# Optimization experiments

Hardware: AMD Instinct MI355X
Metric: run time of the kernel (lower is better)

The kernel has to match this reference:

```python
import jax, jax.numpy as jnp
import numpy as np

N_WORD_IDS, N_TAG_IDS, N_DEPREL_IDS = 100000, 48, 40
N_WORD_F, N_TAG_F, N_DEPREL_F = 18, 18, 12
EMBED, HIDDEN, N_CLASSES = 128, 1024, 3
B = 16384
N_TOTAL = N_WORD_F + N_TAG_F + N_DEPREL_F  # 48


def _he(key, shape):
    fan_in = shape[0]
    return jax.random.normal(key, shape, dtype=jnp.float32) * jnp.sqrt(2.0 / fan_in)


def setup_inputs() -> dict:
    key = jax.random.key(0)
    ks = jax.random.split(key, 8)
    return {
        "word_id_batch": jax.random.randint(ks[0], (B, N_WORD_F), 0, N_WORD_IDS, dtype=jnp.int64 if jax.config.jax_enable_x64 else jnp.int32).astype(jnp.int32),
        "tag_id_batch": jax.random.randint(ks[1], (B, N_TAG_F), 0, N_TAG_IDS).astype(jnp.int32),
        "deprel_id_batch": jax.random.randint(ks[2], (B, N_DEPREL_F), 0, N_DEPREL_IDS).astype(jnp.int32),
        "word_embeddings": jax.random.normal(ks[3], (N_WORD_IDS, EMBED), dtype=jnp.float32) * 0.1,
        "tag_embeddings": _he(ks[4], (N_TAG_IDS, EMBED)),
        "deprel_embeddings": _he(ks[5], (N_DEPREL_IDS, EMBED)),
        "W_h": _he(ks[6], (N_TOTAL * EMBED, HIDDEN)),
        "b_h": jnp.zeros((HIDDEN,), jnp.float32),
        "W_o": _he(ks[7], (HIDDEN, N_CLASSES)),
        "b_o": jnp.zeros((N_CLASSES,), jnp.float32),
    }


def reference(word_id_batch, tag_id_batch, deprel_id_batch,
              word_embeddings, tag_embeddings, deprel_embeddings,
              W_h, b_h, W_o, b_o):
    # one_hot_float(ids) @ E is mathematically a row gather: E[ids]
    b = word_id_batch.shape[0]
    x = jnp.concatenate([
        word_embeddings[word_id_batch].reshape(b, -1),      # (B, 18*E)
        tag_embeddings[tag_id_batch].reshape(b, -1),        # (B, 18*E)
        deprel_embeddings[deprel_id_batch].reshape(b, -1),  # (B, 12*E)
    ], axis=1)                                              # (B, 48*E)
    h = jax.nn.relu(x @ W_h + b_h)
    # dropout is identity in eval mode (self.training == False)
    return h @ W_o + b_o
```

## Files before the change

### kernel.cpp

```cpp
#include <hip/hip_runtime.h>
#include <hip/hip_bf16.h>
#include <cstdint>

typedef unsigned short u16;
typedef __attribute__((ext_vector_type(8))) short bf16x8;
typedef __attribute__((ext_vector_type(4))) float f32x4;

#define B_ROWS 16384
#define N_HID  1024
#define K_DIM  6144
#define EMB    128
#define N_WORD 100000
#define N_TAG  48
#define N_DEP  40
#define NTILES 96
#define NITER  48

__device__ __forceinline__ u16 f2bf(float x) {
  union { float f; uint32_t u; } v; v.f = x;
  uint32_t r = v.u + 0x7fffu + ((v.u >> 16) & 1u);
  return (u16)(r >> 16);
}

__device__ __forceinline__ void gload_lds16(const void* g, void* l) {
  __builtin_amdgcn_global_load_lds(
      (const __attribute__((address_space(1))) void*)g,
      (__attribute__((address_space(3))) void*)l, 16, 0, 0);
}

#define SBAR do { \
  __builtin_amdgcn_sched_barrier(0); \
  asm volatile("" ::: "memory"); \
  __builtin_amdgcn_s_barrier(); \
  asm volatile("" ::: "memory"); \
  __builtin_amdgcn_sched_barrier(0); \
} while (0)

__global__ void init_out_kernel(float* __restrict__ out, const float* __restrict__ b_o) {
  int i = blockIdx.x * blockDim.x + threadIdx.x;
  if (i < B_ROWS * 3) out[i] = b_o[i % 3];
}

__global__ void transpose_wh_kernel(const float* __restrict__ Wh, u16* __restrict__ Wt) {
  __shared__ float tile[32][33];
  int k0 = blockIdx.x * 32, n0 = blockIdx.y * 32;
  int tx = threadIdx.x & 31, ty = threadIdx.x >> 5;
  #pragma unroll
  for (int j = 0; j < 4; ++j)
    tile[ty + j * 8][tx] = Wh[(size_t)(k0 + ty + j * 8) * N_HID + n0 + tx];
  __syncthreads();
  #pragma unroll
  for (int j = 0; j < 4; ++j)
    Wt[(size_t)(n0 + ty + j * 8) * K_DIM + k0 + tx] = f2bf(tile[tx][ty + j * 8]);
}

__global__ void cast_tables_kernel(const float* __restrict__ wordE, const float* __restrict__ tagE,
                                   const float* __restrict__ depE, u16* __restrict__ tblB) {
  const int W8 = N_WORD * EMB / 8, T8 = N_TAG * EMB / 8, D8 = N_DEP * EMB / 8;
  int i = blockIdx.x * blockDim.x + threadIdx.x;
  const float* src; int j;
  if (i < W8)                { src = wordE; j = i; }
  else if (i < W8 + T8)      { src = tagE;  j = i - W8; }
  else if (i < W8 + T8 + D8) { src = depE;  j = i - W8 - T8; }
  else return;
  const float4* s = (const float4*)(src + (size_t)j * 8);
  float4 v0 = s[0], v1 = s[1];
  bf16x8 w;
  w[0] = (short)f2bf(v0.x); w[1] = (short)f2bf(v0.y);
  w[2] = (short)f2bf(v0.z); w[3] = (short)f2bf(v0.w);
  w[4] = (short)f2bf(v1.x); w[5] = (short)f2bf(v1.y);
  w[6] = (short)f2bf(v1.z); w[7] = (short)f2bf(v1.w);
  *(bf16x8*)(tblB + (size_t)i * 8) = w;
}

__global__ void build_offv_kernel(const int* __restrict__ w, const int* __restrict__ t,
                                  const int* __restrict__ d, int* __restrict__ offv) {
  int row = blockIdx.x * 256 + threadIdx.x;
  int f = blockIdx.y;
  if (row >= B_ROWS) return;
  int off;
  if (f < 18)      off = w[row * 18 + f] * EMB;
  else if (f < 36) off = N_WORD * EMB + t[row * 18 + (f - 18)] * EMB;
  else             off = (N_WORD + N_TAG) * EMB + d[row * 12 + (f - 36)] * EMB;
  offv[f * B_ROWS + row] = off;
}

__device__ __forceinline__ void rd_b4(const u16* base, int sch, bf16x8* q) {
  #pragma unroll
  for (int nf = 0; nf < 4; ++nf) q[nf] = *(const bf16x8*)(base + nf * 1024 + sch);
}
__device__ __forceinline__ void rd_a4(const u16* base, int sch, int mh, bf16x8* q) {
  #pragma unroll
  for (int mf = 0; mf < 4; ++mf) q[mf] = *(const bf16x8*)(base + (mh * 4 + mf) * 1024 + sch);
}
__device__ __forceinline__ void mfma16(f32x4 (&acc)[8][4], int mh, const bf16x8* aT, const bf16x8* bq) {
  #pragma unroll
  for (int m = 0; m < 4; ++m)
    #pragma unroll
    for (int n = 0; n < 4; ++n)
      acc[mh * 4 + m][n] = __builtin_amdgcn_mfma_f32_16x16x32_bf16(aT[m], bq[n], acc[mh * 4 + m][n], 0, 0, 0);
}

__global__ __launch_bounds__(512, 2) void fused_v3_kernel(
    const u16* __restrict__ tblB, const int* __restrict__ offv,
    const u16* __restrict__ Wt,   const float* __restrict__ b_h,
    const float* __restrict__ W_o, float* __restrict__ out) {
  __shared__ u16 As[2][256 * 64];
  __shared__ u16 Bs[2][256 * 64];

  const int tid  = threadIdx.x;
  const int lane = tid & 63;
  const int wid  = tid >> 6;
  const int wr   = wid >> 2;
  const int wc   = wid & 3;
  const int bn0  = blockIdx.x * 256;
  const int bm0  = blockIdx.y * 256;
  const int l15  = lane & 15, ca = lane >> 4;

  const int r0 = tid >> 3;
  const int c  = tid & 7;
  const int sc = ((c ^ (r0 & 7)) << 3);
  const u16* Bp[4];
  #pragma unroll
  for (int j = 0; j < 4; ++j)
    Bp[j] = Wt + (size_t)(bn0 + j * 64 + r0) * K_DIM + sc;
  const int ivb = bm0 + r0;

#define DESTA(buf, h, is) ((void*)&As[buf][(h) * 8192 + (is) * 4096 + wid * 512])
#define DESTB(buf, h, is) ((void*)&Bs[buf][(h) * 8192 + (is) * 4096 + wid * 512])
#define STAGE_B2(buf, h, t) do { \
    gload_lds16(Bp[2 * (h)] + (size_t)(t) * 64, DESTB(buf, h, 0)); \
    gload_lds16(Bp[2 * (h) + 1] + (size_t)(t) * 64, DESTB(buf, h, 1)); } while (0)
#define STAGE_A2(buf, h, e0) do { \
    gload_lds16(tblB + (size_t)oA[2 * (h)] + (e0) + sc, DESTA(buf, h, 0)); \
    gload_lds16(tblB + (size_t)oA[2 * (h) + 1] + (e0) + sc, DESTA(buf, h, 1)); } while (0)

  const u16* aBase0 = &As[0][(wr * 128 + l15) * 64];
  const u16* aBase1 = &As[1][(wr * 128 + l15) * 64];
  const u16* bBase0 = &Bs[0][(wc * 64 + l15) * 64];
  const u16* bBase1 = &Bs[1][(wc * 64 + l15) * 64];
  const int sch0 = ((ca    ) ^ (l15 & 7)) << 3;
  const int sch1 = ((ca + 4) ^ (l15 & 7)) << 3;

  f32x4 acc[8][4] = {};
  int oA[4];

  STAGE_B2(0, 0, 0); STAGE_B2(0, 1, 0);
  #pragma unroll
  for (int j = 0; j < 4; ++j) oA[j] = offv[ivb + j * 64];
  STAGE_A2(0, 0, 0); STAGE_A2(0, 1, 0);
  STAGE_B2(1, 0, 1); STAGE_B2(1, 1, 1);
  asm volatile("s_waitcnt vmcnt(4)" ::: "memory");
  SBAR;

  #pragma unroll 1
  for (int i = 0; i < NITER; ++i) {
    const int T = 2 * i;
    bf16x8 bq0[4], bq1[4], aT[4];
    rd_b4(bBase0, sch0, bq0);
    rd_a4(aBase0, sch0, 0, aT);
    STAGE_A2(1, 0, 64);
    SBAR;
    __builtin_amdgcn_s_setprio(1); mfma16(acc, 0, aT, bq0); __builtin_amdgcn_s_setprio(0);
    SBAR;
    rd_b4(bBase0, sch1, bq1);
    rd_a4(aBase0, sch0, 1, aT);
    STAGE_A2(1, 1, 64);
    SBAR;
    __builtin_amdgcn_s_setprio(1); mfma16(acc, 1, aT, bq0); __builtin_amdgcn_s_setprio(0);
    SBAR;
    if (i + 1 < NITER) {
      const int* ov = offv + (i + 1) * B_ROWS + ivb;
      #pragma unroll
      for (int j = 0; j < 4; ++j) oA[j] = ov[j * 64];
    }
    rd_a4(aBase0, sch1, 0, aT);
    if (T + 2 < NTILES) STAGE_B2(0, 0, T + 2);
    SBAR;
    __builtin_amdgcn_s_setprio(1); mfma16(acc, 0, aT, bq1); __builtin_amdgcn_s_setprio(0);
    SBAR;
    rd_a4(aBase0, sch1, 1, aT);
    if (T + 2 < NTILES) STAGE_B2(0, 1, T + 2);
    if (i == NITER - 1) { asm volatile("s_waitcnt vmcnt(0)" ::: "memory"); }
    else                { asm volatile("s_waitcnt vmcnt(8)" ::: "memory"); }
    SBAR;
    __builtin_amdgcn_s_setprio(1); mfma16(acc, 1, aT, bq1); __builtin_amdgcn_s_setprio(0);
    SBAR;
    rd_b4(bBase1, sch0, bq0);
    rd_a4(aBase1, sch0, 0, aT);
    if (T + 2 < NTILES) STAGE_A2(0, 0, 0);
    SBAR;
    __builtin_amdgcn_s_setprio(1); mfma16(acc, 0, aT, bq0); __builtin_amdgcn_s_setprio(0);
    SBAR;
    rd_b4(bBase1, sch1, bq1);
    rd_a4(aBase1, sch0, 1, aT);
    if (T + 2 < NTILES) STAGE_A2(0, 1, 0);
    SBAR;
    __builtin_amdgcn_s_setprio(1); mfma16(acc, 1, aT, bq0); __builtin_amdgcn_s_setprio(0);
    SBAR;
    rd_a4(aBase1, sch1, 0, aT);
    if (T + 3 < NTILES) STAGE_B2(1, 0, T + 3);
    SBAR;
    __builtin_amdgcn_s_setprio(1); mfma16(acc, 0, aT, bq1); __builtin_amdgcn_s_setprio(0);
    SBAR;
    rd_a4(aBase1, sch1, 1, aT);
    if (T + 3 < NTILES) STAGE_B2(1, 1, T + 3);
    asm volatile("s_waitcnt vmcnt(4)" ::: "memory");
    SBAR;
    __builtin_amdgcn_s_setprio(1); mfma16(acc, 1, aT, bq1); __builtin_amdgcn_s_setprio(0);
    SBAR;
  }

  float bh[4], wo[4][3];
  #pragma unroll
  for (int nf = 0; nf < 4; ++nf) {
    int j = bn0 + wc * 64 + nf * 16 + l15;
    bh[nf] = b_h[j];
    wo[nf][0] = W_o[j * 3 + 0]; wo[nf][1] = W_o[j * 3 + 1]; wo[nf][2] = W_o[j * 3 + 2];
  }
  #pragma unroll
  for (int mf = 0; mf < 8; ++mf) {
    #pragma unroll
    for (int reg = 0; reg < 4; ++reg) {
      float p0 = 0.f, p1 = 0.f, p2 = 0.f;
      #pragma unroll
      for (int nf = 0; nf < 4; ++nf) {
        float h = acc[mf][nf][reg] + bh[nf];
        h = fmaxf(h, 0.f);
        p0 += h * wo[nf][0]; p1 += h * wo[nf][1]; p2 += h * wo[nf][2];
      }
      #pragma unroll
      for (int mask = 1; mask < 16; mask <<= 1) {
        p0 += __shfl_xor(p0, mask);
        p1 += __shfl_xor(p1, mask);
        p2 += __shfl_xor(p2, mask);
      }
      if (l15 == 0) {
        int row = bm0 + wr * 128 + mf * 16 + (ca << 2) + reg;
        atomicAdd(&out[row * 3 + 0], p0);
        atomicAdd(&out[row * 3 + 1], p1);
        atomicAdd(&out[row * 3 + 2], p2);
      }
    }
  }
#undef DESTA
#undef DESTB
#undef STAGE_B2
#undef STAGE_A2
}

__global__ __launch_bounds__(256, 4) void fused_v2_kernel(
    const int* __restrict__ word_ids, const int* __restrict__ tag_ids,
    const int* __restrict__ dep_ids,  const u16* __restrict__ tblB,
    const u16* __restrict__ Wt,       const float* __restrict__ b_h,
    const float* __restrict__ W_o,    float* __restrict__ out) {
  __shared__ u16 As2[128 * 64];
  __shared__ u16 Bs2[128 * 64];
  const int tid  = threadIdx.x;
  const int lane = tid & 63;
  const int wid  = tid >> 6;
  const int wr   = wid >> 1, wc = wid & 1;
  const int bm0  = blockIdx.y * 128;
  const int bn0  = blockIdx.x * 128;
  f32x4 acc[4][4] = {};

  for (int kt = 0; kt < K_DIM / 64; ++kt) {
    __syncthreads();
    {
      int f = kt >> 1, e0 = (kt & 1) << 6;
      const int* ids; int nf, fl; size_t tb;
      if (f < 18)      { ids = word_ids; nf = 18; fl = f;      tb = 0; }
      else if (f < 36) { ids = tag_ids;  nf = 18; fl = f - 18; tb = (size_t)N_WORD * EMB; }
      else             { ids = dep_ids;  nf = 12; fl = f - 36; tb = (size_t)(N_WORD + N_TAG) * EMB; }
      #pragma unroll
      for (int it = 0; it < 4; ++it) {
        int cidx = wid * 256 + it * 64 + lane;
        int r = cidx >> 3, cc = cidx & 7;
        int id = ids[(bm0 + r) * nf + fl];
        const u16* src = tblB + tb + (size_t)id * EMB + e0 + ((cc ^ (r & 7)) << 3);
        gload_lds16(src, &As2[(wid * 256 + it * 64) * 8]);
      }
    }
    #pragma unroll
    for (int it = 0; it < 4; ++it) {
      int cidx = wid * 256 + it * 64 + lane;
      int rn = cidx >> 3, cc = cidx & 7;
      const u16* src = Wt + (size_t)(bn0 + rn) * K_DIM + kt * 64 + ((cc ^ (rn & 7)) << 3);
      gload_lds16(src, &Bs2[(wid * 256 + it * 64) * 8]);
    }
    __syncthreads();
    const int l15 = lane & 15, ca = lane >> 4;
    #pragma unroll
    for (int ks = 0; ks < 2; ++ks) {
      bf16x8 a[4], b[4];
      #pragma unroll
      for (int m = 0; m < 4; ++m) {
        int ra = wr * 64 + m * 16 + l15;
        int ch = (ca + ks * 4) ^ (ra & 7);
        a[m] = *(const bf16x8*)&As2[ra * 64 + ch * 8];
      }
      #pragma unroll
      for (int n = 0; n < 4; ++n) {
        int rb = wc * 64 + n * 16 + l15;
        int ch = (ca + ks * 4) ^ (rb & 7);
        b[n] = *(const bf16x8*)&Bs2[rb * 64 + ch * 8];
      }
      #pragma unroll
      for (int m = 0; m < 4; ++m)
        #pragma unroll
        for (int n = 0; n < 4; ++n)
          acc[m][n] = __builtin_amdgcn_mfma_f32_16x16x32_bf16(a[m], b[n], acc[m][n], 0, 0, 0);
    }
  }

  const int l15 = lane & 15;
  float bh[4], wo[4][3];
  #pragma unroll
  for (int n = 0; n < 4; ++n) {
    int j = bn0 + wc * 64 + n * 16 + l15;
    bh[n] = b_h[j];
    wo[n][0] = W_o[j * 3 + 0]; wo[n][1] = W_o[j * 3 + 1]; wo[n][2] = W_o[j * 3 + 2];
  }
  #pragma unroll
  for (int m = 0; m < 4; ++m) {
    #pragma unroll
    for (int reg = 0; reg < 4; ++reg) {
      float p0 = 0.f, p1 = 0.f, p2 = 0.f;
      #pragma unroll
      for (int n = 0; n < 4; ++n) {
        float h = acc[m][n][reg] + bh[n];
        h = fmaxf(h, 0.f);
        p0 += h * wo[n][0]; p1 += h * wo[n][1]; p2 += h * wo[n][2];
      }
      #pragma unroll
      for (int mask = 1; mask < 16; mask <<= 1) {
        p0 += __shfl_xor(p0, mask);
        p1 += __shfl_xor(p1, mask);
        p2 += __shfl_xor(p2, mask);
      }
      if (l15 == 0) {
        int row = bm0 + wr * 64 + m * 16 + ((lane >> 4) << 2) + reg;
        atomicAdd(&out[row * 3 + 0], p0);
        atomicAdd(&out[row * 3 + 1], p1);
        atomicAdd(&out[row * 3 + 2], p2);
      }
    }
  }
}

extern "C" void kernel_launch(void* const* d_in, const int* in_sizes, int n_in,
                              void* d_out, int out_size, void* d_ws, size_t ws_size,
                              hipStream_t stream) {
  const int*   word_ids = (const int*)d_in[0];
  const int*   tag_ids  = (const int*)d_in[1];
  const int*   dep_ids  = (const int*)d_in[2];
  const float* wordE    = (const float*)d_in[3];
  const float* tagE     = (const float*)d_in[4];
  const float* depE     = (const float*)d_in[5];
  const float* Wh       = (const float*)d_in[6];
  const float* b_h      = (const float*)d_in[7];
  const float* W_o      = (const float*)d_in[8];
  const float* b_o      = (const float*)d_in[9];
  float*       out      = (float*)d_out;

  const size_t WT_ELEMS  = (size_t)N_HID * K_DIM;
  const size_t TBL_ELEMS = (size_t)(N_WORD + N_TAG + N_DEP) * EMB;
  const size_t OFFV_ELEMS = (size_t)48 * B_ROWS;
  const size_t NEED_V2 = (WT_ELEMS + TBL_ELEMS) * sizeof(u16);
  const size_t NEED_V3 = NEED_V2 + OFFV_ELEMS * sizeof(int);

  u16* Wt   = (u16*)d_ws;
  u16* tblB = Wt + WT_ELEMS;
  int* offv = (int*)(tblB + TBL_ELEMS);

  init_out_kernel<<<(B_ROWS * 3 + 255) / 256, 256, 0, stream>>>(out, b_o);

  if (d_ws && ws_size >= NEED_V3) {
    transpose_wh_kernel<<<dim3(K_DIM / 32, N_HID / 32), 256, 0, stream>>>(Wh, Wt);
    cast_tables_kernel<<<(int)((TBL_ELEMS / 8 + 255) / 256), 256, 0, stream>>>(wordE, tagE, depE, tblB);
    build_offv_kernel<<<dim3(B_ROWS / 256, 48), 256, 0, stream>>>(word_ids, tag_ids, dep_ids, offv);
    fused_v3_kernel<<<dim3(N_HID / 256, B_ROWS / 256), 512, 0, stream>>>(
        tblB, offv, Wt, b_h, W_o, out);
  } else if (d_ws && ws_size >= NEED_V2) {
    transpose_wh_kernel<<<dim3(K_DIM / 32, N_HID / 32), 256, 0, stream>>>(Wh, Wt);
    cast_tables_kernel<<<(int)((TBL_ELEMS / 8 + 255) / 256), 256, 0, stream>>>(wordE, tagE, depE, tblB);
    fused_v2_kernel<<<dim3(N_HID / 128, B_ROWS / 128), 256, 0, stream>>>(
        word_ids, tag_ids, dep_ids, tblB, Wt, b_h, W_o, out);
  }
}
```

Measured before the change: 325.1 us.

## Switch fused GEMM to 32x32x16 MFMA with register double-buffered LDS reads

Replaces the 16x16x32 bf16 MFMA tiling with 32x32x16 MFMA (4x2 fragments per wave), which halves the number of LDS fragment reads per unit of compute and issues fewer, larger matrix instructions. The pipeline is restructured so LDS fragment reads for the next k-slice are double-buffered in registers while the current MFMAs run, and A and B global staging for the next tile are issued together. The epilogue is adapted to the 32x32 output layout, with wider shuffle reductions. Risks include higher register pressure and a less staggered global prefetch with a full vmcnt(0) wait each iteration.

Measured after the change: 381.3 us. 1.17x slower.

```diff
diff --git a/kernel.cpp b/kernel.cpp
--- a/kernel.cpp
+++ b/kernel.cpp
@@ -5,6 +5,7 @@
 typedef unsigned short u16;
 typedef __attribute__((ext_vector_type(8))) short bf16x8;
 typedef __attribute__((ext_vector_type(4))) float f32x4;
+typedef __attribute__((ext_vector_type(16))) float f32x16;
 
 #define B_ROWS 16384
 #define N_HID  1024
@@ -85,23 +86,7 @@
   offv[f * B_ROWS + row] = off;
 }
 
-__device__ __forceinline__ void rd_b4(const u16* base, int sch, bf16x8* q) {
-  #pragma unroll
-  for (int nf = 0; nf < 4; ++nf) q[nf] = *(const bf16x8*)(base + nf * 1024 + sch);
-}
-__device__ __forceinline__ void rd_a4(const u16* base, int sch, int mh, bf16x8* q) {
-  #pragma unroll
-  for (int mf = 0; mf < 4; ++mf) q[mf] = *(const bf16x8*)(base + (mh * 4 + mf) * 1024 + sch);
-}
-__device__ __forceinline__ void mfma16(f32x4 (&acc)[8][4], int mh, const bf16x8* aT, const bf16x8* bq) {
-  #pragma unroll
-  for (int m = 0; m < 4; ++m)
-    #pragma unroll
-    for (int n = 0; n < 4; ++n)
-      acc[mh * 4 + m][n] = __builtin_amdgcn_mfma_f32_16x16x32_bf16(aT[m], bq[n], acc[mh * 4 + m][n], 0, 0, 0);
-}
-
-__global__ __launch_bounds__(512, 2) void fused_v3_kernel(
+__global__ __launch_bounds__(512, 2) void fused_v4_kernel(
     const u16* __restrict__ tblB, const int* __restrict__ offv,
     const u16* __restrict__ Wt,   const float* __restrict__ b_h,
     const float* __restrict__ W_o, float* __restrict__ out) {
@@ -115,7 +100,7 @@
   const int wc   = wid & 3;
   const int bn0  = blockIdx.x * 256;
   const int bm0  = blockIdx.y * 256;
-  const int l15  = lane & 15, ca = lane >> 4;
+  const int l31  = lane & 31, lh = lane >> 5;
 
   const int r0 = tid >> 3;
   const int c  = tid & 7;
@@ -135,108 +120,113 @@
     gload_lds16(tblB + (size_t)oA[2 * (h)] + (e0) + sc, DESTA(buf, h, 0)); \
     gload_lds16(tblB + (size_t)oA[2 * (h) + 1] + (e0) + sc, DESTA(buf, h, 1)); } while (0)
 
-  const u16* aBase0 = &As[0][(wr * 128 + l15) * 64];
-  const u16* aBase1 = &As[1][(wr * 128 + l15) * 64];
-  const u16* bBase0 = &Bs[0][(wc * 64 + l15) * 64];
-  const u16* bBase1 = &Bs[1][(wc * 64 + l15) * 64];
-  const int sch0 = ((ca    ) ^ (l15 & 7)) << 3;
-  const int sch1 = ((ca + 4) ^ (l15 & 7)) << 3;
-
-  f32x4 acc[8][4] = {};
+  const u16* aB[2] = { &As[0][(wr * 128 + l31) * 64], &As[1][(wr * 128 + l31) * 64] };
+  const u16* bB[2] = { &Bs[0][(wc * 64  + l31) * 64], &Bs[1][(wc * 64  + l31) * 64] };
+  int sch[4];
+  #pragma unroll
+  for (int ks = 0; ks < 4; ++ks) sch[ks] = (((ks * 2 + lh) ^ (lane & 7)) << 3);
+
+#define RD(Aset, Bset, buf, ks) do { \
+    _Pragma("unroll") for (int mf = 0; mf < 4; ++mf) \
+      Aset[mf] = *(const bf16x8*)(aB[buf] + mf * 2048 + sch[ks]); \
+    _Pragma("unroll") for (int nf = 0; nf < 2; ++nf) \
+      Bset[nf] = *(const bf16x8*)(bB[buf] + nf * 2048 + sch[ks]); } while (0)
+
+#define MM(Aset, Bset) do { \
+    __builtin_amdgcn_s_setprio(1); \
+    _Pragma("unroll") for (int mf = 0; mf < 4; ++mf) \
+      _Pragma("unroll") for (int nf = 0; nf < 2; ++nf) \
+        acc[mf][nf] = __builtin_amdgcn_mfma_f32_32x32x16_bf16(Aset[mf], Bset[nf], acc[mf][nf], 0, 0, 0); \
+    __builtin_amdgcn_s_setprio(0); } while (0)
+
+  f32x16 acc[4][2] = {};
   int oA[4];
+  bf16x8 A0[4], A1[4], B0[2], B1[2];
 
   STAGE_B2(0, 0, 0); STAGE_B2(0, 1, 0);
   #pragma unroll
   for (int j = 0; j < 4; ++j) oA[j] = offv[ivb + j * 64];
   STAGE_A2(0, 0, 0); STAGE_A2(0, 1, 0);
-  STAGE_B2(1, 0, 1); STAGE_B2(1, 1, 1);
-  asm volatile("s_waitcnt vmcnt(4)" ::: "memory");
+  asm volatile("s_waitcnt vmcnt(0)" ::: "memory");
   SBAR;
+  RD(A0, B0, 0, 0);
 
   #pragma unroll 1
   for (int i = 0; i < NITER; ++i) {
     const int T = 2 * i;
-    bf16x8 bq0[4], bq1[4], aT[4];
-    rd_b4(bBase0, sch0, bq0);
-    rd_a4(aBase0, sch0, 0, aT);
-    STAGE_A2(1, 0, 64);
-    SBAR;
-    __builtin_amdgcn_s_setprio(1); mfma16(acc, 0, aT, bq0); __builtin_amdgcn_s_setprio(0);
-    SBAR;
-    rd_b4(bBase0, sch1, bq1);
-    rd_a4(aBase0, sch0, 1, aT);
-    STAGE_A2(1, 1, 64);
-    SBAR;
-    __builtin_amdgcn_s_setprio(1); mfma16(acc, 1, aT, bq0); __builtin_amdgcn_s_setprio(0);
-    SBAR;
-    if (i + 1 < NITER) {
+    const bool more = (i + 1 < NITER);
+    RD(A1, B1, 0, 1);
+    STAGE_A2(1, 0, 64); STAGE_B2(1, 0, T + 1);
+    SBAR;
+    MM(A0, B0);
+    SBAR;
+    RD(A0, B0, 0, 2);
+    STAGE_A2(1, 1, 64); STAGE_B2(1, 1, T + 1);
+    SBAR;
+    MM(A1, B1);
+    SBAR;
+    if (more) {
       const int* ov = offv + (i + 1) * B_ROWS + ivb;
       #pragma unroll
       for (int j = 0; j < 4; ++j) oA[j] = ov[j * 64];
     }
-    rd_a4(aBase0, sch1, 0, aT);
-    if (T + 2 < NTILES) STAGE_B2(0, 0, T + 2);
-    SBAR;
-    __builtin_amdgcn_s_setprio(1); mfma16(acc, 0, aT, bq1); __builtin_amdgcn_s_setprio(0);
-    SBAR;
-    rd_a4(aBase0, sch1, 1, aT);
-    if (T + 2 < NTILES) STAGE_B2(0, 1, T + 2);
+    RD(A1, B1, 0, 3);
+    SBAR;
+    MM(A0, B0);
+    SBAR;
     if (i == NITER - 1) { asm volatile("s_waitcnt vmcnt(0)" ::: "memory"); }
-    else                { asm volatile("s_waitcnt vmcnt(8)" ::: "memory"); }
-    SBAR;
-    __builtin_amdgcn_s_setprio(1); mfma16(acc, 1, aT, bq1); __builtin_amdgcn_s_setprio(0);
-    SBAR;
-    rd_b4(bBase1, sch0, bq0);
-    rd_a4(aBase1, sch0, 0, aT);
-    if (T + 2 < NTILES) STAGE_A2(0, 0, 0);
-    SBAR;
-    __builtin_amdgcn_s_setprio(1); mfma16(acc, 0, aT, bq0); __builtin_amdgcn_s_setprio(0);
-    SBAR;
-    rd_b4(bBase1, sch1, bq1);
-    rd_a4(aBase1, sch0, 1, aT);
-    if (T + 2 < NTILES) STAGE_A2(0, 1, 0);
-    SBAR;
-    __builtin_amdgcn_s_setprio(1); mfma16(acc, 1, aT, bq0); __builtin_amdgcn_s_setprio(0);
-    SBAR;
-    rd_a4(aBase1, sch1, 0, aT);
-    if (T + 3 < NTILES) STAGE_B2(1, 0, T + 3);
-    SBAR;
-    __builtin_amdgcn_s_setprio(1); mfma16(acc, 0, aT, bq1); __builtin_amdgcn_s_setprio(0);
-    SBAR;
-    rd_a4(aBase1, sch1, 1, aT);
-    if (T + 3 < NTILES) STAGE_B2(1, 1, T + 3);
-    asm volatile("s_waitcnt vmcnt(4)" ::: "memory");
-    SBAR;
-    __builtin_amdgcn_s_setprio(1); mfma16(acc, 1, aT, bq1); __builtin_amdgcn_s_setprio(0);
-    SBAR;
-  }
-
-  float bh[4], wo[4][3];
-  #pragma unroll
-  for (int nf = 0; nf < 4; ++nf) {
-    int j = bn0 + wc * 64 + nf * 16 + l15;
+    else                { asm volatile("s_waitcnt vmcnt(4)" ::: "memory"); }
+    SBAR;
+    RD(A0, B0, 1, 0);
+    MM(A1, B1);
+    SBAR;
+    RD(A1, B1, 1, 1);
+    if (more) { STAGE_A2(0, 0, 0); STAGE_B2(0, 0, T + 2); }
+    SBAR;
+    MM(A0, B0);
+    SBAR;
+    RD(A0, B0, 1, 2);
+    if (more) { STAGE_A2(0, 1, 0); STAGE_B2(0, 1, T + 2); }
+    SBAR;
+    MM(A1, B1);
+    SBAR;
+    RD(A1, B1, 1, 3);
+    SBAR;
+    MM(A0, B0);
+    SBAR;
+    if (more) { asm volatile("s_waitcnt vmcnt(0)" ::: "memory"); }
+    SBAR;
+    if (more) RD(A0, B0, 0, 0);
+    MM(A1, B1);
+    SBAR;
+  }
+
+  float bh[2], wo[2][3];
+  #pragma unroll
+  for (int nf = 0; nf < 2; ++nf) {
+    int j = bn0 + wc * 64 + nf * 32 + l31;
     bh[nf] = b_h[j];
     wo[nf][0] = W_o[j * 3 + 0]; wo[nf][1] = W_o[j * 3 + 1]; wo[nf][2] = W_o[j * 3 + 2];
   }
   #pragma unroll
-  for (int mf = 0; mf < 8; ++mf) {
+  for (int mf = 0; mf < 4; ++mf) {
     #pragma unroll
-    for (int reg = 0; reg < 4; ++reg) {
+    for (int reg = 0; reg < 16; ++reg) {
       float p0 = 0.f, p1 = 0.f, p2 = 0.f;
       #pragma unroll
-      for (int nf = 0; nf < 4; ++nf) {
+      for (int nf = 0; nf < 2; ++nf) {
         float h = acc[mf][nf][reg] + bh[nf];
         h = fmaxf(h, 0.f);
         p0 += h * wo[nf][0]; p1 += h * wo[nf][1]; p2 += h * wo[nf][2];
       }
       #pragma unroll
-      for (int mask = 1; mask < 16; mask <<= 1) {
+      for (int mask = 1; mask < 32; mask <<= 1) {
         p0 += __shfl_xor(p0, mask);
         p1 += __shfl_xor(p1, mask);
         p2 += __shfl_xor(p2, mask);
       }
-      if (l15 == 0) {
-        int row = bm0 + wr * 128 + mf * 16 + (ca << 2) + reg;
+      if (l31 == 0) {
+        int row = bm0 + wr * 128 + mf * 32 + (reg & 3) + 8 * (reg >> 2) + 4 * lh;
         atomicAdd(&out[row * 3 + 0], p0);
         atomicAdd(&out[row * 3 + 1], p1);
         atomicAdd(&out[row * 3 + 2], p2);
@@ -247,6 +237,8 @@
 #undef DESTB
 #undef STAGE_B2
 #undef STAGE_A2
+#undef RD
+#undef MM
 }
 
 __global__ __launch_bounds__(256, 4) void fused_v2_kernel(
@@ -363,11 +355,11 @@
   const float* b_o      = (const float*)d_in[9];
   float*       out      = (float*)d_out;
 
-  const size_t WT_ELEMS  = (size_t)N_HID * K_DIM;
-  const size_t TBL_ELEMS = (size_t)(N_WORD + N_TAG + N_DEP) * EMB;
+  const size_t WT_ELEMS   = (size_t)N_HID * K_DIM;
+  const size_t TBL_ELEMS  = (size_t)(N_WORD + N_TAG + N_DEP) * EMB;
   const size_t OFFV_ELEMS = (size_t)48 * B_ROWS;
   const size_t NEED_V2 = (WT_ELEMS + TBL_ELEMS) * sizeof(u16);
-  const size_t NEED_V3 = NEED_V2 + OFFV_ELEMS * sizeof(int);
+  const size_t NEED_V4 = NEED_V2 + OFFV_ELEMS * sizeof(int);
 
   u16* Wt   = (u16*)d_ws;
   u16* tblB = Wt + WT_ELEMS;
@@ -375,11 +367,11 @@
 
   init_out_kernel<<<(B_ROWS * 3 + 255) / 256, 256, 0, stream>>>(out, b_o);
 
-  if (d_ws && ws_size >= NEED_V3) {
+  if (d_ws && ws_size >= NEED_V4) {
     transpose_wh_kernel<<<dim3(K_DIM / 32, N_HID / 32), 256, 0, stream>>>(Wh, Wt);
     cast_tables_kernel<<<(int)((TBL_ELEMS / 8 + 255) / 256), 256, 0, stream>>>(wordE, tagE, depE, tblB);
     build_offv_kernel<<<dim3(B_ROWS / 256, 48), 256, 0, stream>>>(word_ids, tag_ids, dep_ids, offv);
-    fused_v3_kernel<<<dim3(N_HID / 256, B_ROWS / 256), 512, 0, stream>>>(
+    fused_v4_kernel<<<dim3(N_HID / 256, B_ROWS / 256), 512, 0, stream>>>(
         tblB, offv, Wt, b_h, W_o, out);
   } else if (d_ws && ws_size >= NEED_V2) {
     transpose_wh_kernel<<<dim3(K_DIM / 32, N_HID / 32), 256, 0, stream>>>(Wh, Wt);
```

## Software-pipeline LDS fragment reads and reschedule global staging in fused GEMM loop

Applied to the files above, without the earlier changes.

Restructures the main K loop so LDS-to-register fragment reads for the next MFMA block use double register sets (aT0/aT1, bq0/bq1) and are issued before the current MFMAs. B tiles are now staged together with A tiles, and the waitcnt placement changes accordingly. Launch bounds drop to one block per SIMD set, which frees registers for the extra fragments but may lower occupancy. The aim is to hide LDS read latency behind MFMA work, at the cost of more register pressure and a changed global-load overlap depth.

Result: slower. 528.8 us (+62.6%).

```diff
diff --git a/kernel.cpp b/kernel.cpp
--- a/kernel.cpp
+++ b/kernel.cpp
@@ -94,14 +94,16 @@
   for (int mf = 0; mf < 4; ++mf) q[mf] = *(const bf16x8*)(base + (mh * 4 + mf) * 1024 + sch);
 }
 __device__ __forceinline__ void mfma16(f32x4 (&acc)[8][4], int mh, const bf16x8* aT, const bf16x8* bq) {
+  __builtin_amdgcn_s_setprio(1);
   #pragma unroll
   for (int m = 0; m < 4; ++m)
     #pragma unroll
     for (int n = 0; n < 4; ++n)
       acc[mh * 4 + m][n] = __builtin_amdgcn_mfma_f32_16x16x32_bf16(aT[m], bq[n], acc[mh * 4 + m][n], 0, 0, 0);
-}
-
-__global__ __launch_bounds__(512, 2) void fused_v3_kernel(
+  __builtin_amdgcn_s_setprio(0);
+}
+
+__global__ __launch_bounds__(512, 1) void fused_v5_kernel(
     const u16* __restrict__ tblB, const int* __restrict__ offv,
     const u16* __restrict__ Wt,   const float* __restrict__ b_h,
     const float* __restrict__ W_o, float* __restrict__ out) {
@@ -144,70 +146,70 @@
 
   f32x4 acc[8][4] = {};
   int oA[4];
+  bf16x8 aT0[4], aT1[4], bq0[4], bq1[4];
 
   STAGE_B2(0, 0, 0); STAGE_B2(0, 1, 0);
   #pragma unroll
   for (int j = 0; j < 4; ++j) oA[j] = offv[ivb + j * 64];
   STAGE_A2(0, 0, 0); STAGE_A2(0, 1, 0);
-  STAGE_B2(1, 0, 1); STAGE_B2(1, 1, 1);
-  asm volatile("s_waitcnt vmcnt(4)" ::: "memory");
+  asm volatile("s_waitcnt vmcnt(0)" ::: "memory");
   SBAR;
+  rd_b4(bBase0, sch0, bq0);
+  rd_a4(aBase0, sch0, 0, aT0);
 
   #pragma unroll 1
   for (int i = 0; i < NITER; ++i) {
     const int T = 2 * i;
-    bf16x8 bq0[4], bq1[4], aT[4];
-    rd_b4(bBase0, sch0, bq0);
-    rd_a4(aBase0, sch0, 0, aT);
-    STAGE_A2(1, 0, 64);
-    SBAR;
-    __builtin_amdgcn_s_setprio(1); mfma16(acc, 0, aT, bq0); __builtin_amdgcn_s_setprio(0);
-    SBAR;
+    const bool more = (i + 1 < NITER);
+    rd_a4(aBase0, sch0, 1, aT1);
     rd_b4(bBase0, sch1, bq1);
-    rd_a4(aBase0, sch0, 1, aT);
-    STAGE_A2(1, 1, 64);
-    SBAR;
-    __builtin_amdgcn_s_setprio(1); mfma16(acc, 1, aT, bq0); __builtin_amdgcn_s_setprio(0);
-    SBAR;
-    if (i + 1 < NITER) {
+    STAGE_A2(1, 0, 64); STAGE_B2(1, 0, T + 1);
+    SBAR;
+    mfma16(acc, 0, aT0, bq0);
+    SBAR;
+    rd_a4(aBase0, sch1, 0, aT0);
+    STAGE_A2(1, 1, 64); STAGE_B2(1, 1, T + 1);
+    SBAR;
+    mfma16(acc, 1, aT1, bq0);
+    SBAR;
+    rd_a4(aBase0, sch1, 1, aT1);
+    if (more) {
       const int* ov = offv + (i + 1) * B_ROWS + ivb;
       #pragma unroll
       for (int j = 0; j < 4; ++j) oA[j] = ov[j * 64];
     }
-    rd_a4(aBase0, sch1, 0, aT);
-    if (T + 2 < NTILES) STAGE_B2(0, 0, T + 2);
-    SBAR;
-    __builtin_amdgcn_s_setprio(1); mfma16(acc, 0, aT, bq1); __builtin_amdgcn_s_setprio(0);
-    SBAR;
-    rd_a4(aBase0, sch1, 1, aT);
-    if (T + 2 < NTILES) STAGE_B2(0, 1, T + 2);
-    if (i == NITER - 1) { asm volatile("s_waitcnt vmcnt(0)" ::: "memory"); }
-    else                { asm volatile("s_waitcnt vmcnt(8)" ::: "memory"); }
-    SBAR;
-    __builtin_amdgcn_s_setprio(1); mfma16(acc, 1, aT, bq1); __builtin_amdgcn_s_setprio(0);
+    SBAR;
+    mfma16(acc, 0, aT0, bq1);
+    SBAR;
+    if (more) { asm volatile("s_waitcnt vmcnt(4)" ::: "memory"); }
+    else      { asm volatile("s_waitcnt vmcnt(0)" ::: "memory"); }
     SBAR;
     rd_b4(bBase1, sch0, bq0);
-    rd_a4(aBase1, sch0, 0, aT);
-    if (T + 2 < NTILES) STAGE_A2(0, 0, 0);
-    SBAR;
-    __builtin_amdgcn_s_setprio(1); mfma16(acc, 0, aT, bq0); __builtin_amdgcn_s_setprio(0);
-    SBAR;
+    rd_a4(aBase1, sch0, 0, aT0);
+    mfma16(acc, 1, aT1, bq1);
+    SBAR;
+    rd_a4(aBase1, sch0, 1, aT1);
     rd_b4(bBase1, sch1, bq1);
-    rd_a4(aBase1, sch0, 1, aT);
-    if (T + 2 < NTILES) STAGE_A2(0, 1, 0);
-    SBAR;
-    __builtin_amdgcn_s_setprio(1); mfma16(acc, 1, aT, bq0); __builtin_amdgcn_s_setprio(0);
-    SBAR;
-    rd_a4(aBase1, sch1, 0, aT);
-    if (T + 3 < NTILES) STAGE_B2(1, 0, T + 3);
-    SBAR;
-    __builtin_amdgcn_s_setprio(1); mfma16(acc, 0, aT, bq1); __builtin_amdgcn_s_setprio(0);
-    SBAR;
-    rd_a4(aBase1, sch1, 1, aT);
-    if (T + 3 < NTILES) STAGE_B2(1, 1, T + 3);
-    asm volatile("s_waitcnt vmcnt(4)" ::: "memory");
-    SBAR;
-    __builtin_amdgcn_s_setprio(1); mfma16(acc, 1, aT, bq1); __builtin_amdgcn_s_setprio(0);
+    if (more) { STAGE_A2(0, 0, 0); STAGE_B2(0, 0, T + 2); }
+    SBAR;
+    mfma16(acc, 0, aT0, bq0);
+    SBAR;
+    rd_a4(aBase1, sch1, 0, aT0);
+    if (more) { STAGE_A2(0, 1, 0); STAGE_B2(0, 1, T + 2); }
+    SBAR;
+    mfma16(acc, 1, aT1, bq0);
+    SBAR;
+    rd_a4(aBase1, sch1, 1, aT1);
+    SBAR;
+    mfma16(acc, 0, aT0, bq1);
+    SBAR;
+    if (more) { asm volatile("s_waitcnt vmcnt(0)" ::: "memory"); }
+    SBAR;
+    if (more) {
+      rd_b4(bBase0, sch0, bq0);
+      rd_a4(aBase0, sch0, 0, aT0);
+    }
+    mfma16(acc, 1, aT1, bq1);
     SBAR;
   }
 
@@ -363,11 +365,11 @@
   const float* b_o      = (const float*)d_in[9];
   float*       out      = (float*)d_out;
 
-  const size_t WT_ELEMS  = (size_t)N_HID * K_DIM;
-  const size_t TBL_ELEMS = (size_t)(N_WORD + N_TAG + N_DEP) * EMB;
+  const size_t WT_ELEMS   = (size_t)N_HID * K_DIM;
+  const size_t TBL_ELEMS  = (size_t)(N_WORD + N_TAG + N_DEP) * EMB;
   const size_t OFFV_ELEMS = (size_t)48 * B_ROWS;
   const size_t NEED_V2 = (WT_ELEMS + TBL_ELEMS) * sizeof(u16);
-  const size_t NEED_V3 = NEED_V2 + OFFV_ELEMS * sizeof(int);
+  const size_t NEED_V5 = NEED_V2 + OFFV_ELEMS * sizeof(int);
 
   u16* Wt   = (u16*)d_ws;
   u16* tblB = Wt + WT_ELEMS;
@@ -375,11 +377,11 @@
 
   init_out_kernel<<<(B_ROWS * 3 + 255) / 256, 256, 0, stream>>>(out, b_o);
 
-  if (d_ws && ws_size >= NEED_V3) {
+  if (d_ws && ws_size >= NEED_V5) {
     transpose_wh_kernel<<<dim3(K_DIM / 32, N_HID / 32), 256, 0, stream>>>(Wh, Wt);
     cast_tables_kernel<<<(int)((TBL_ELEMS / 8 + 255) / 256), 256, 0, stream>>>(wordE, tagE, depE, tblB);
     build_offv_kernel<<<dim3(B_ROWS / 256, 48), 256, 0, stream>>>(word_ids, tag_ids, dep_ids, offv);
-    fused_v3_kernel<<<dim3(N_HID / 256, B_ROWS / 256), 512, 0, stream>>>(
+    fused_v5_kernel<<<dim3(N_HID / 256, B_ROWS / 256), 512, 0, stream>>>(
         tblB, offv, Wt, b_h, W_o, out);
   } else if (d_ws && ws_size >= NEED_V2) {
     transpose_wh_kernel<<<dim3(K_DIM / 32, N_HID / 32), 256, 0, stream>>>(Wh, Wt);
```
